# Optimization experiments

Hardware: AMD Instinct MI355X
Metric: run time of the kernel (lower is better)

Reference implementation:

```python
import jax, jax.numpy as jnp
import numpy as np

IN_C, OUT_C = 32, 64
KSIZE = (3, 3, 3)


def setup_inputs() -> dict:
    key = jax.random.key(0)
    k1, k2 = jax.random.split(key)
    x = jax.random.normal(k1, (2, IN_C, 64, 64, 64), dtype=jnp.float32)
    # One learnable scalar per (out_channel, in_channel, kz, ky, kx) basis function.
    W = jax.random.normal(k2, (OUT_C, IN_C) + KSIZE, dtype=jnp.float32) * 0.05
    return {"x": x, "W": W}


def reference(x, W):
    # Original: for each (oc, ic, kz, ky, kx), out[:, oc] += basis(x[:, ic, shifted_slices])
    # With scalar-weight bases this is exactly a VALID (unpadded) 3D convolution:
    # out[b, o, d, h, w] = sum_{i, kz, ky, kx} W[o, i, kz, ky, kx] * x[b, i, d+kz, h+ky, w+kx]
    return jax.lax.conv_general_dilated(
        x, W,
        window_strides=(1, 1, 1),
        padding="VALID",
        dimension_numbers=("NCDHW", "OIDHW", "NCDHW"),
    )
```

## Files before the change

kernel.cpp:

```cpp
#include <hip/hip_runtime.h>
#include <hip/hip_bf16.h>

#define DIN 64
#define DOUT 62
#define ICH 32
#define OCH 64

typedef __bf16 bf16x8 __attribute__((ext_vector_type(8)));
typedef float f32x4 __attribute__((ext_vector_type(4)));
typedef float f32x8 __attribute__((ext_vector_type(8)));
typedef float f32x16 __attribute__((ext_vector_type(16)));

#define AS1U(p) ((const __attribute__((address_space(1))) unsigned int*)(p))
#define AS3U(p) ((__attribute__((address_space(3))) unsigned int*)(p))

__global__ void prep_w(const float* __restrict__ W, unsigned short* __restrict__ Wre3) {
    int idx = blockIdx.x * 256 + threadIdx.x;
    if (idx >= 27 * OCH * ICH) return;
    int j    = idx & 7;
    int lane = (idx >> 3) & 63;
    int kh   = (idx >> 9) & 1;
    int mt   = (idx >> 10) & 1;
    int tap  = idx >> 11;
    int oc   = mt * 32 + (lane & 31);
    int ic   = kh * 16 + (lane >> 5) * 8 + j;
    float v  = W[((size_t)oc * ICH + ic) * 27 + tap];
    Wre3[idx] = __builtin_bit_cast(unsigned short, (__bf16)v);
}

__global__ void prep_x(const float* __restrict__ x, unsigned short* __restrict__ xp) {
    int idx = blockIdx.x * 256 + threadIdx.x;
    int w = idx & 63;
    int s = (idx >> 6) & 3;
    int y = (idx >> 8) & 63;
    int z = (idx >> 14) & 63;
    int b = idx >> 20;
    const float* xb = x + ((size_t)(b * ICH + s * 8)) * 262144 + (size_t)z * 4096 + y * 64 + w;
    bf16x8 pk;
#pragma unroll
    for (int j = 0; j < 8; ++j)
        pk[j] = (__bf16)xb[(size_t)j * 262144];
    ((int4*)xp)[idx] = __builtin_bit_cast(int4, pk);
}

__global__ __launch_bounds__(512, 4) void conv3d_mfma_pk(
    const unsigned short* __restrict__ Wre3,
    const unsigned short* __restrict__ xp,
    float* __restrict__ out)
{
    __shared__ char xs[2][40960];

    const int tid  = threadIdx.x;
    const int lane = tid & 63;
    const int wave = tid >> 6;

    const int orig = blockIdx.x;
    const int lid  = (orig & 7) * 124 + (orig >> 3);
    const int ht = lid & 7;
    const int rr = lid >> 3;
    const int d  = rr % DOUT;
    const int b  = rr / DOUT;
    const int h0 = ht * 8;

    const int l31 = lane & 31;
    const int lhi = lane >> 5;
    const int row = wave;

    auto stage_chunk = [&](char* buf, int z, int i) {
        int c  = wave * 5 + i;
        int yl = c >> 2;
        int sl = c & 3;
        int srow = h0 + yl; if (srow > 63) srow = 63;
        const unsigned short* src =
            xp + ((((size_t)(b * DIN + z) * DIN + srow) * 4 + sl) * 64) * 8 + lane * 8;
        __builtin_amdgcn_global_load_lds(AS1U(src), AS3U(buf + c * 1024), 16, 0, 0);
    };
    auto loadA = [&](int tap, int4* af) {
        const int4* wp = (const int4*)Wre3 + (size_t)tap * 256 + lane;
#pragma unroll
        for (int q = 0; q < 4; ++q)
            af[q] = wp[q * 64];
    };
    auto readB = [&](const char* buf, int ky, int kx, int4* dst) {
#pragma unroll
        for (int kh = 0; kh < 2; ++kh) {
            const int g = kh * 2 + lhi;
#pragma unroll
            for (int nt = 0; nt < 2; ++nt) {
                int wb = nt * 32 + l31 + kx;
                if (wb > 63) wb = 63;
                dst[kh * 2 + nt] = *(const int4*)(buf + (((row + ky) * 4 + g) * 64 + wb) * 16);
            }
        }
    };

#pragma unroll
    for (int i = 0; i < 5; ++i) stage_chunk(xs[0], d, i);
    int4 af[2][4];
    loadA(0, af[0]);

    f32x16 acc[2][2];
#pragma unroll
    for (int mt = 0; mt < 2; ++mt)
#pragma unroll
        for (int nt = 0; nt < 2; ++nt)
#pragma unroll
            for (int r = 0; r < 16; ++r) acc[mt][nt][r] = 0.f;

    __syncthreads();

#pragma unroll
    for (int kz = 0; kz < 3; ++kz) {
        char* cur = xs[kz & 1];
        char* nxt = xs[(kz + 1) & 1];

#pragma unroll
        for (int t = 0; t < 9; ++t) {
            const int T = kz * 9 + t;
            int4 bfr[4];
            readB(cur, t / 3, t % 3, bfr);
            if (T < 26) loadA(T + 1, af[(T + 1) & 1]);
            if (kz < 2 && t < 5) stage_chunk(nxt, d + kz + 1, t);

            __builtin_amdgcn_s_setprio(1);
#pragma unroll
            for (int kh = 0; kh < 2; ++kh)
#pragma unroll
                for (int mt = 0; mt < 2; ++mt)
#pragma unroll
                    for (int nt = 0; nt < 2; ++nt)
                        acc[mt][nt] = __builtin_amdgcn_mfma_f32_32x32x16_bf16(
                            __builtin_bit_cast(bf16x8, af[T & 1][mt * 2 + kh]),
                            __builtin_bit_cast(bf16x8, bfr[kh * 2 + nt]),
                            acc[mt][nt], 0, 0, 0);
            __builtin_amdgcn_s_setprio(0);
        }
        if (kz < 2) __syncthreads();
    }

    const int h = h0 + row;
    if (h < DOUT) {
#pragma unroll
        for (int mt = 0; mt < 2; ++mt) {
#pragma unroll
            for (int r = 0; r < 16; ++r) {
                int oc = mt * 32 + (r & 3) + 8 * (r >> 2) + 4 * lhi;
                size_t ob = ((((size_t)b * OCH + oc) * DOUT + d) * DOUT + h) * DOUT;
#pragma unroll
                for (int nt = 0; nt < 2; ++nt) {
                    int ww = nt * 32 + l31;
                    if (ww < DOUT) out[ob + ww] = acc[mt][nt][r];
                }
            }
        }
    }
}

__global__ __launch_bounds__(256, 3) void conv3d_mfma_fb(
    const float* __restrict__ x, const float* __restrict__ W,
    float* __restrict__ out)
{
    __shared__ char xs[2][6 * 66 * 64];

    const int tid  = threadIdx.x;
    const int lane = tid & 63;
    const int wave = tid >> 6;

    const int orig = blockIdx.x;
    const int lid  = (orig & 7) * 248 + (orig >> 3);
    const int ht = lid & 15;
    const int rr = lid >> 4;
    const int d  = rr % DOUT;
    const int b  = rr / DOUT;
    const int h0 = ht * 4;

    const int wlo = lane & 15;
    const int whi = lane >> 4;
    const int row = wave;

    const int icg  = wave;
    const int w    = lane;
    const int slot = icg ^ ((w >> 1) & 3);

    auto issueRow = [&](int z, int y) -> f32x8 {
        int gy = h0 + y; if (gy > 63) gy = 63;
        const float* xp2 = x + (((size_t)(b * ICH + icg * 8) * DIN + z) * DIN + gy) * DIN + w;
        f32x8 s;
#pragma unroll
        for (int j = 0; j < 8; ++j) s[j] = xp2[(size_t)j * DIN * DIN * DIN];
        return s;
    };
    auto writeRow = [&](char* buf, int y, f32x8 s) {
        bf16x8 pk;
#pragma unroll
        for (int j = 0; j < 8; ++j) pk[j] = (__bf16)s[j];
        *(int4*)(buf + ((y * 66 + w) * 64 + slot * 16)) = __builtin_bit_cast(int4, pk);
    };
    auto loadA = [&](int tap, int4* af) {
#pragma unroll
        for (int mt = 0; mt < 4; ++mt) {
            const float* wp = W + ((size_t)(mt * 16 + wlo) * ICH + whi * 8) * 27 + tap;
            bf16x8 t;
#pragma unroll
            for (int j = 0; j < 8; ++j) t[j] = (__bf16)wp[j * 27];
            af[mt] = __builtin_bit_cast(int4, t);
        }
    };
    auto readB = [&](const char* buf, int ky, int kx, int4* dst) {
#pragma unroll
        for (int nt = 0; nt < 4; ++nt) {
            int wb = nt * 16 + wlo + kx;
            int sl = whi ^ ((wb >> 1) & 3);
            dst[nt] = *(const int4*)(buf + (((row + ky) * 66 + wb) * 64 + sl * 16));
        }
    };

    if (tid < 96) {
        int bu = tid / 48, q2 = tid % 48;
        int y = q2 >> 3, q = q2 & 7;
        int w2 = 64 + (q >> 2), sl = q & 3;
        *(int4*)(xs[bu] + ((y * 66 + w2) * 64 + sl * 16)) = int4{0, 0, 0, 0};
    }
    {
        f32x8 s0 = issueRow(d, 0), s1 = issueRow(d, 1), s2 = issueRow(d, 2);
        writeRow(xs[0], 0, s0); s0 = issueRow(d, 3);
        writeRow(xs[0], 1, s1); s1 = issueRow(d, 4);
        writeRow(xs[0], 2, s2); s2 = issueRow(d, 5);
        writeRow(xs[0], 3, s0); writeRow(xs[0], 4, s1); writeRow(xs[0], 5, s2);
    }
    int4 af[2][4];
    loadA(0, af[0]);
    __syncthreads();

    f32x4 acc[4][4];
#pragma unroll
    for (int mt = 0; mt < 4; ++mt)
#pragma unroll
        for (int nt = 0; nt < 4; ++nt)
            acc[mt][nt] = f32x4{0.f, 0.f, 0.f, 0.f};

    int4 bfr[2][4];

#pragma unroll
    for (int kz = 0; kz < 3; ++kz) {
        char* cur = xs[kz & 1];
        char* nxt = xs[(kz + 1) & 1];
        f32x8 s0, s1, s2;
        readB(cur, 0, 0, bfr[0]);
#pragma unroll
        for (int t = 0; t < 9; ++t) {
            const int T = kz * 9 + t;
            if (T < 26) loadA(T + 1, af[(T + 1) & 1]);
            if (t < 8)  readB(cur, (t + 1) / 3, (t + 1) % 3, bfr[(t + 1) & 1]);
            if (kz < 2) {
                if (t == 3) writeRow(nxt, 0, s0);
                if (t == 4) writeRow(nxt, 1, s1);
                if (t == 5) writeRow(nxt, 2, s2);
                if (t == 6) writeRow(nxt, 3, s0);
                if (t == 7) writeRow(nxt, 4, s1);
                if (t == 8) writeRow(nxt, 5, s2);
                if (t == 0) s0 = issueRow(d + kz + 1, 0);
                if (t == 1) s1 = issueRow(d + kz + 1, 1);
                if (t == 2) s2 = issueRow(d + kz + 1, 2);
                if (t == 3) s0 = issueRow(d + kz + 1, 3);
                if (t == 4) s1 = issueRow(d + kz + 1, 4);
                if (t == 5) s2 = issueRow(d + kz + 1, 5);
            }
#pragma unroll
            for (int mt = 0; mt < 4; ++mt)
#pragma unroll
                for (int nt = 0; nt < 4; ++nt)
                    acc[mt][nt] = __builtin_amdgcn_mfma_f32_16x16x32_bf16(
                        __builtin_bit_cast(bf16x8, af[T & 1][mt]),
                        __builtin_bit_cast(bf16x8, bfr[t & 1][nt]),
                        acc[mt][nt], 0, 0, 0);
        }
        if (kz < 2) __syncthreads();
    }

    const int h = h0 + row;
    if (h < DOUT) {
#pragma unroll
        for (int mt = 0; mt < 4; ++mt) {
#pragma unroll
            for (int r = 0; r < 4; ++r) {
                int oc = mt * 16 + whi * 4 + r;
                size_t ob = ((((size_t)b * OCH + oc) * DOUT + d) * DOUT + h) * DOUT;
#pragma unroll
                for (int nt = 0; nt < 4; ++nt) {
                    int ww = nt * 16 + wlo;
                    if (ww < DOUT) out[ob + ww] = acc[mt][nt][r];
                }
            }
        }
    }
}

extern "C" void kernel_launch(void* const* d_in, const int* in_sizes, int n_in,
                              void* d_out, int out_size, void* d_ws, size_t ws_size,
                              hipStream_t stream) {
    const float* x = (const float*)d_in[0];
    const float* W = (const float*)d_in[1];
    float* out = (float*)d_out;

    const size_t wre_elems = (size_t)27 * OCH * ICH;
    const size_t xp_elems  = (size_t)2 * DIN * DIN * DIN * ICH;
    const size_t need = (wre_elems + xp_elems) * 2 + 256;

    if (ws_size >= need) {
        unsigned short* Wre3 = (unsigned short*)d_ws;
        unsigned short* xp   = Wre3 + wre_elems;
        prep_w<<<216, 256, 0, stream>>>(W, Wre3);
        prep_x<<<8192, 256, 0, stream>>>(x, xp);
        conv3d_mfma_pk<<<dim3(2 * DOUT * 8), 512, 0, stream>>>(Wre3, xp, out);
    } else {
        conv3d_mfma_fb<<<dim3(2 * DOUT * 16), 256, 0, stream>>>(x, W, out);
    }
}
```

Before: 90.26 us.

## Halve per-block tile to 4 rows, split width across waves, double-buffer B reads

Each block now covers 4 output rows instead of 8, with the 8 waves split into 4 rows by 2 width halves. That halves the per-wave accumulators and B registers, cuts LDS per block from 80KB to 48KB, and doubles the grid, with launch bounds raised to allow more resident blocks per CU. It also prefetches the next tap's B fragments into a double buffer so LDS reads overlap the MFMAs. The cost is more halo rows staged per output row (6 rows per 4 outputs instead of 10 per 8) and each weight fragment is reused across only one width tile per wave.

```diff
diff --git a/kernel.cpp b/kernel.cpp
--- a/kernel.cpp
+++ b/kernel.cpp
@@ -43,31 +43,32 @@
     ((int4*)xp)[idx] = __builtin_bit_cast(int4, pk);
 }
 
-__global__ __launch_bounds__(512, 4) void conv3d_mfma_pk(
+__global__ __launch_bounds__(512, 6) void conv3d_mfma_pk(
     const unsigned short* __restrict__ Wre3,
     const unsigned short* __restrict__ xp,
     float* __restrict__ out)
 {
-    __shared__ char xs[2][40960];
+    __shared__ char xs[2][24576];
 
     const int tid  = threadIdx.x;
     const int lane = tid & 63;
     const int wave = tid >> 6;
+    const int row  = wave & 3;
+    const int whalf= wave >> 2;
 
     const int orig = blockIdx.x;
-    const int lid  = (orig & 7) * 124 + (orig >> 3);
-    const int ht = lid & 7;
-    const int rr = lid >> 3;
+    const int lid  = (orig & 7) * 248 + (orig >> 3);
+    const int ht = lid & 15;
+    const int rr = lid >> 4;
     const int d  = rr % DOUT;
     const int b  = rr / DOUT;
-    const int h0 = ht * 8;
+    const int h0 = ht * 4;
 
     const int l31 = lane & 31;
     const int lhi = lane >> 5;
-    const int row = wave;
 
     auto stage_chunk = [&](char* buf, int z, int i) {
-        int c  = wave * 5 + i;
+        int c  = wave * 3 + i;
         int yl = c >> 2;
         int sl = c & 3;
         int srow = h0 + yl; if (srow > 63) srow = 63;
@@ -82,75 +83,66 @@
             af[q] = wp[q * 64];
     };
     auto readB = [&](const char* buf, int ky, int kx, int4* dst) {
+        int wb = whalf * 32 + l31 + kx;
+        if (wb > 63) wb = 63;
 #pragma unroll
         for (int kh = 0; kh < 2; ++kh) {
             const int g = kh * 2 + lhi;
-#pragma unroll
-            for (int nt = 0; nt < 2; ++nt) {
-                int wb = nt * 32 + l31 + kx;
-                if (wb > 63) wb = 63;
-                dst[kh * 2 + nt] = *(const int4*)(buf + (((row + ky) * 4 + g) * 64 + wb) * 16);
-            }
-        }
-    };
-
-#pragma unroll
-    for (int i = 0; i < 5; ++i) stage_chunk(xs[0], d, i);
+            dst[kh] = *(const int4*)(buf + (((row + ky) * 4 + g) * 64 + wb) * 16);
+        }
+    };
+
+#pragma unroll
+    for (int i = 0; i < 3; ++i) stage_chunk(xs[0], d, i);
     int4 af[2][4];
     loadA(0, af[0]);
 
-    f32x16 acc[2][2];
+    f32x16 acc[2];
 #pragma unroll
     for (int mt = 0; mt < 2; ++mt)
 #pragma unroll
-        for (int nt = 0; nt < 2; ++nt)
-#pragma unroll
-            for (int r = 0; r < 16; ++r) acc[mt][nt][r] = 0.f;
+        for (int r = 0; r < 16; ++r) acc[mt][r] = 0.f;
 
     __syncthreads();
+
+    int4 bfr[2][2];
 
 #pragma unroll
     for (int kz = 0; kz < 3; ++kz) {
         char* cur = xs[kz & 1];
         char* nxt = xs[(kz + 1) & 1];
+        readB(cur, 0, 0, bfr[0]);
 
 #pragma unroll
         for (int t = 0; t < 9; ++t) {
             const int T = kz * 9 + t;
-            int4 bfr[4];
-            readB(cur, t / 3, t % 3, bfr);
             if (T < 26) loadA(T + 1, af[(T + 1) & 1]);
-            if (kz < 2 && t < 5) stage_chunk(nxt, d + kz + 1, t);
+            if (t < 8)  readB(cur, (t + 1) / 3, (t + 1) % 3, bfr[(t + 1) & 1]);
+            if (kz < 2 && t < 3) stage_chunk(nxt, d + kz + 1, t);
 
             __builtin_amdgcn_s_setprio(1);
 #pragma unroll
             for (int kh = 0; kh < 2; ++kh)
 #pragma unroll
                 for (int mt = 0; mt < 2; ++mt)
-#pragma unroll
-                    for (int nt = 0; nt < 2; ++nt)
-                        acc[mt][nt] = __builtin_amdgcn_mfma_f32_32x32x16_bf16(
-                            __builtin_bit_cast(bf16x8, af[T & 1][mt * 2 + kh]),
-                            __builtin_bit_cast(bf16x8, bfr[kh * 2 + nt]),
-                            acc[mt][nt], 0, 0, 0);
+                    acc[mt] = __builtin_amdgcn_mfma_f32_32x32x16_bf16(
+                        __builtin_bit_cast(bf16x8, af[T & 1][mt * 2 + kh]),
+                        __builtin_bit_cast(bf16x8, bfr[t & 1][kh]),
+                        acc[mt], 0, 0, 0);
             __builtin_amdgcn_s_setprio(0);
         }
         if (kz < 2) __syncthreads();
     }
 
     const int h = h0 + row;
-    if (h < DOUT) {
+    const int ww = whalf * 32 + l31;
+    if (h < DOUT && ww < DOUT) {
 #pragma unroll
         for (int mt = 0; mt < 2; ++mt) {
 #pragma unroll
             for (int r = 0; r < 16; ++r) {
                 int oc = mt * 32 + (r & 3) + 8 * (r >> 2) + 4 * lhi;
-                size_t ob = ((((size_t)b * OCH + oc) * DOUT + d) * DOUT + h) * DOUT;
-#pragma unroll
-                for (int nt = 0; nt < 2; ++nt) {
-                    int ww = nt * 32 + l31;
-                    if (ww < DOUT) out[ob + ww] = acc[mt][nt][r];
-                }
+                out[((((size_t)b * OCH + oc) * DOUT + d) * DOUT + h) * DOUT + ww] = acc[mt][r];
             }
         }
     }
@@ -312,7 +304,7 @@
         unsigned short* xp   = Wre3 + wre_elems;
         prep_w<<<216, 256, 0, stream>>>(W, Wre3);
         prep_x<<<8192, 256, 0, stream>>>(x, xp);
-        conv3d_mfma_pk<<<dim3(2 * DOUT * 8), 512, 0, stream>>>(Wre3, xp, out);
+        conv3d_mfma_pk<<<dim3(2 * DOUT * 16), 512, 0, stream>>>(Wre3, xp, out);
     } else {
         conv3d_mfma_fb<<<dim3(2 * DOUT * 16), 256, 0, stream>>>(x, W, out);
     }
```

Result: slower. 300.0 us (+232.4%).

## Drop LDS staging; read conv input directly from global with register prefetch

Applied to the files above, without the earlier changes.

Removes the double-buffered LDS staging of input rows via global_load_lds and the block barriers. Each wave now loads its B fragments directly from the packed bf16 input in global memory, prefetching two taps ahead in a 3-deep register ring. Blocks shrink to 256 threads covering 4 output rows, with twice as many blocks. This is meant to eliminate barrier stalls and LDS traffic, at the cost of redundant global and L2 reads across overlapping rows and taps, and higher register pressure.

```diff
diff --git a/kernel.cpp b/kernel.cpp
--- a/kernel.cpp
+++ b/kernel.cpp
@@ -10,9 +10,6 @@
 typedef float f32x4 __attribute__((ext_vector_type(4)));
 typedef float f32x8 __attribute__((ext_vector_type(8)));
 typedef float f32x16 __attribute__((ext_vector_type(16)));
-
-#define AS1U(p) ((const __attribute__((address_space(1))) unsigned int*)(p))
-#define AS3U(p) ((__attribute__((address_space(3))) unsigned int*)(p))
 
 __global__ void prep_w(const float* __restrict__ W, unsigned short* __restrict__ Wre3) {
     int idx = blockIdx.x * 256 + threadIdx.x;
@@ -43,61 +40,51 @@
     ((int4*)xp)[idx] = __builtin_bit_cast(int4, pk);
 }
 
-__global__ __launch_bounds__(512, 4) void conv3d_mfma_pk(
+__global__ __launch_bounds__(256, 3) void conv3d_mfma_pk(
     const unsigned short* __restrict__ Wre3,
     const unsigned short* __restrict__ xp,
     float* __restrict__ out)
 {
-    __shared__ char xs[2][40960];
-
     const int tid  = threadIdx.x;
     const int lane = tid & 63;
     const int wave = tid >> 6;
 
     const int orig = blockIdx.x;
-    const int lid  = (orig & 7) * 124 + (orig >> 3);
-    const int ht = lid & 7;
-    const int rr = lid >> 3;
+    const int lid  = (orig & 7) * 248 + (orig >> 3);
+    const int ht = lid & 15;
+    const int rr = lid >> 4;
     const int d  = rr % DOUT;
     const int b  = rr / DOUT;
-    const int h0 = ht * 8;
+    const int h0 = ht * 4;
 
     const int l31 = lane & 31;
     const int lhi = lane >> 5;
     const int row = wave;
 
-    auto stage_chunk = [&](char* buf, int z, int i) {
-        int c  = wave * 5 + i;
-        int yl = c >> 2;
-        int sl = c & 3;
-        int srow = h0 + yl; if (srow > 63) srow = 63;
-        const unsigned short* src =
-            xp + ((((size_t)(b * DIN + z) * DIN + srow) * 4 + sl) * 64) * 8 + lane * 8;
-        __builtin_amdgcn_global_load_lds(AS1U(src), AS3U(buf + c * 1024), 16, 0, 0);
-    };
     auto loadA = [&](int tap, int4* af) {
         const int4* wp = (const int4*)Wre3 + (size_t)tap * 256 + lane;
 #pragma unroll
         for (int q = 0; q < 4; ++q)
             af[q] = wp[q * 64];
     };
-    auto readB = [&](const char* buf, int ky, int kx, int4* dst) {
+    auto readB = [&](int z, int ky, int kx, int4* dst) {
+        int y = h0 + row + ky; if (y > 63) y = 63;
+        const int4* base = (const int4*)xp + ((((size_t)b * DIN + z) * DIN + y) * 4) * 64;
+        int w0 = l31 + kx;
+        int w1 = 32 + l31 + kx; if (w1 > 63) w1 = 63;
 #pragma unroll
         for (int kh = 0; kh < 2; ++kh) {
             const int g = kh * 2 + lhi;
-#pragma unroll
-            for (int nt = 0; nt < 2; ++nt) {
-                int wb = nt * 32 + l31 + kx;
-                if (wb > 63) wb = 63;
-                dst[kh * 2 + nt] = *(const int4*)(buf + (((row + ky) * 4 + g) * 64 + wb) * 16);
-            }
-        }
-    };
-
-#pragma unroll
-    for (int i = 0; i < 5; ++i) stage_chunk(xs[0], d, i);
+            dst[kh * 2 + 0] = base[g * 64 + w0];
+            dst[kh * 2 + 1] = base[g * 64 + w1];
+        }
+    };
+
     int4 af[2][4];
+    int4 bfr[3][4];
     loadA(0, af[0]);
+    readB(d, 0, 0, bfr[0]);
+    readB(d, 0, 1, bfr[1]);
 
     f32x16 acc[2][2];
 #pragma unroll
@@ -107,35 +94,26 @@
 #pragma unroll
             for (int r = 0; r < 16; ++r) acc[mt][nt][r] = 0.f;
 
-    __syncthreads();
-
-#pragma unroll
-    for (int kz = 0; kz < 3; ++kz) {
-        char* cur = xs[kz & 1];
-        char* nxt = xs[(kz + 1) & 1];
-
-#pragma unroll
-        for (int t = 0; t < 9; ++t) {
-            const int T = kz * 9 + t;
-            int4 bfr[4];
-            readB(cur, t / 3, t % 3, bfr);
-            if (T < 26) loadA(T + 1, af[(T + 1) & 1]);
-            if (kz < 2 && t < 5) stage_chunk(nxt, d + kz + 1, t);
-
-            __builtin_amdgcn_s_setprio(1);
-#pragma unroll
-            for (int kh = 0; kh < 2; ++kh)
-#pragma unroll
-                for (int mt = 0; mt < 2; ++mt)
-#pragma unroll
-                    for (int nt = 0; nt < 2; ++nt)
-                        acc[mt][nt] = __builtin_amdgcn_mfma_f32_32x32x16_bf16(
-                            __builtin_bit_cast(bf16x8, af[T & 1][mt * 2 + kh]),
-                            __builtin_bit_cast(bf16x8, bfr[kh * 2 + nt]),
-                            acc[mt][nt], 0, 0, 0);
-            __builtin_amdgcn_s_setprio(0);
-        }
-        if (kz < 2) __syncthreads();
+#pragma unroll
+    for (int T = 0; T < 27; ++T) {
+        if (T < 26) loadA(T + 1, af[(T + 1) & 1]);
+        if (T < 25) {
+            const int Tn = T + 2;
+            readB(d + Tn / 9, (Tn % 9) / 3, Tn % 3, bfr[Tn % 3]);
+        }
+
+        __builtin_amdgcn_s_setprio(1);
+#pragma unroll
+        for (int kh = 0; kh < 2; ++kh)
+#pragma unroll
+            for (int mt = 0; mt < 2; ++mt)
+#pragma unroll
+                for (int nt = 0; nt < 2; ++nt)
+                    acc[mt][nt] = __builtin_amdgcn_mfma_f32_32x32x16_bf16(
+                        __builtin_bit_cast(bf16x8, af[T & 1][mt * 2 + kh]),
+                        __builtin_bit_cast(bf16x8, bfr[T % 3][kh * 2 + nt]),
+                        acc[mt][nt], 0, 0, 0);
+        __builtin_amdgcn_s_setprio(0);
     }
 
     const int h = h0 + row;
@@ -312,7 +290,7 @@
         unsigned short* xp   = Wre3 + wre_elems;
         prep_w<<<216, 256, 0, stream>>>(W, Wre3);
         prep_x<<<8192, 256, 0, stream>>>(x, xp);
-        conv3d_mfma_pk<<<dim3(2 * DOUT * 8), 512, 0, stream>>>(Wre3, xp, out);
+        conv3d_mfma_pk<<<dim3(2 * DOUT * 16), 256, 0, stream>>>(Wre3, xp, out);
     } else {
         conv3d_mfma_fb<<<dim3(2 * DOUT * 16), 256, 0, stream>>>(x, W, out);
     }
```

After: 139.4 us. 54.4% more time.

## Compute two output rows per wave to reuse weight fragments across rows

Applied to the files above, without the earlier changes.

Halves the block to 4 waves, and each wave now computes two adjacent output rows. Each weight A-fragment load therefore feeds twice as many MFMAs, which halves global weight-load traffic per output. Each wave stages 10 input chunks instead of 5, and the s_setprio hints are removed. The cost is double the accumulator registers (64 f32x16 values' worth), which lowers occupancy to the declared 2 blocks of 256 per CU, and fewer waves are available to hide latency.

```diff
diff --git a/kernel.cpp b/kernel.cpp
--- a/kernel.cpp
+++ b/kernel.cpp
@@ -43,7 +43,7 @@
     ((int4*)xp)[idx] = __builtin_bit_cast(int4, pk);
 }
 
-__global__ __launch_bounds__(512, 4) void conv3d_mfma_pk(
+__global__ __launch_bounds__(256, 2) void conv3d_mfma_pk(
     const unsigned short* __restrict__ Wre3,
     const unsigned short* __restrict__ xp,
     float* __restrict__ out)
@@ -64,10 +64,10 @@
 
     const int l31 = lane & 31;
     const int lhi = lane >> 5;
-    const int row = wave;
+    const int row0 = wave * 2;
 
     auto stage_chunk = [&](char* buf, int z, int i) {
-        int c  = wave * 5 + i;
+        int c  = wave * 10 + i;
         int yl = c >> 2;
         int sl = c & 3;
         int srow = h0 + yl; if (srow > 63) srow = 63;
@@ -81,7 +81,7 @@
         for (int q = 0; q < 4; ++q)
             af[q] = wp[q * 64];
     };
-    auto readB = [&](const char* buf, int ky, int kx, int4* dst) {
+    auto readB = [&](const char* buf, int yloc, int kx, int4* dst) {
 #pragma unroll
         for (int kh = 0; kh < 2; ++kh) {
             const int g = kh * 2 + lhi;
@@ -89,25 +89,29 @@
             for (int nt = 0; nt < 2; ++nt) {
                 int wb = nt * 32 + l31 + kx;
                 if (wb > 63) wb = 63;
-                dst[kh * 2 + nt] = *(const int4*)(buf + (((row + ky) * 4 + g) * 64 + wb) * 16);
-            }
-        }
-    };
-
-#pragma unroll
-    for (int i = 0; i < 5; ++i) stage_chunk(xs[0], d, i);
+                dst[kh * 2 + nt] = *(const int4*)(buf + ((yloc * 4 + g) * 64 + wb) * 16);
+            }
+        }
+    };
+
+#pragma unroll
+    for (int i = 0; i < 10; ++i) stage_chunk(xs[0], d, i);
     int4 af[2][4];
     loadA(0, af[0]);
 
-    f32x16 acc[2][2];
-#pragma unroll
-    for (int mt = 0; mt < 2; ++mt)
-#pragma unroll
-        for (int nt = 0; nt < 2; ++nt)
-#pragma unroll
-            for (int r = 0; r < 16; ++r) acc[mt][nt][r] = 0.f;
+    f32x16 acc[2][2][2];
+#pragma unroll
+    for (int r2 = 0; r2 < 2; ++r2)
+#pragma unroll
+        for (int mt = 0; mt < 2; ++mt)
+#pragma unroll
+            for (int nt = 0; nt < 2; ++nt)
+#pragma unroll
+                for (int r = 0; r < 16; ++r) acc[r2][mt][nt][r] = 0.f;
 
     __syncthreads();
+
+    int4 bfr0[4], bfr1[4];
 
 #pragma unroll
     for (int kz = 0; kz < 3; ++kz) {
@@ -116,40 +120,56 @@
 
 #pragma unroll
         for (int t = 0; t < 9; ++t) {
-            const int T = kz * 9 + t;
-            int4 bfr[4];
-            readB(cur, t / 3, t % 3, bfr);
+            const int T  = kz * 9 + t;
+            const int ky = t / 3, kx = t % 3;
+
+            readB(cur, row0 + ky, kx, bfr0);
             if (T < 26) loadA(T + 1, af[(T + 1) & 1]);
-            if (kz < 2 && t < 5) stage_chunk(nxt, d + kz + 1, t);
-
-            __builtin_amdgcn_s_setprio(1);
+            if (kz < 2) {
+                if (t == 0) { stage_chunk(nxt, d + kz + 1, 0); stage_chunk(nxt, d + kz + 1, 1); }
+                else        { stage_chunk(nxt, d + kz + 1, t + 1); }
+            }
+            readB(cur, row0 + 1 + ky, kx, bfr1);
+
 #pragma unroll
             for (int kh = 0; kh < 2; ++kh)
 #pragma unroll
                 for (int mt = 0; mt < 2; ++mt)
 #pragma unroll
                     for (int nt = 0; nt < 2; ++nt)
-                        acc[mt][nt] = __builtin_amdgcn_mfma_f32_32x32x16_bf16(
+                        acc[0][mt][nt] = __builtin_amdgcn_mfma_f32_32x32x16_bf16(
                             __builtin_bit_cast(bf16x8, af[T & 1][mt * 2 + kh]),
-                            __builtin_bit_cast(bf16x8, bfr[kh * 2 + nt]),
-                            acc[mt][nt], 0, 0, 0);
-            __builtin_amdgcn_s_setprio(0);
+                            __builtin_bit_cast(bf16x8, bfr0[kh * 2 + nt]),
+                            acc[0][mt][nt], 0, 0, 0);
+#pragma unroll
+            for (int kh = 0; kh < 2; ++kh)
+#pragma unroll
+                for (int mt = 0; mt < 2; ++mt)
+#pragma unroll
+                    for (int nt = 0; nt < 2; ++nt)
+                        acc[1][mt][nt] = __builtin_amdgcn_mfma_f32_32x32x16_bf16(
+                            __builtin_bit_cast(bf16x8, af[T & 1][mt * 2 + kh]),
+                            __builtin_bit_cast(bf16x8, bfr1[kh * 2 + nt]),
+                            acc[1][mt][nt], 0, 0, 0);
         }
         if (kz < 2) __syncthreads();
     }
 
-    const int h = h0 + row;
-    if (h < DOUT) {
-#pragma unroll
-        for (int mt = 0; mt < 2; ++mt) {
-#pragma unroll
-            for (int r = 0; r < 16; ++r) {
-                int oc = mt * 32 + (r & 3) + 8 * (r >> 2) + 4 * lhi;
-                size_t ob = ((((size_t)b * OCH + oc) * DOUT + d) * DOUT + h) * DOUT;
-#pragma unroll
-                for (int nt = 0; nt < 2; ++nt) {
-                    int ww = nt * 32 + l31;
-                    if (ww < DOUT) out[ob + ww] = acc[mt][nt][r];
+#pragma unroll
+    for (int r2 = 0; r2 < 2; ++r2) {
+        const int h = h0 + row0 + r2;
+        if (h < DOUT) {
+#pragma unroll
+            for (int mt = 0; mt < 2; ++mt) {
+#pragma unroll
+                for (int r = 0; r < 16; ++r) {
+                    int oc = mt * 32 + (r & 3) + 8 * (r >> 2) + 4 * lhi;
+                    size_t ob = ((((size_t)b * OCH + oc) * DOUT + d) * DOUT + h) * DOUT;
+#pragma unroll
+                    for (int nt = 0; nt < 2; ++nt) {
+                        int ww = nt * 32 + l31;
+                        if (ww < DOUT) out[ob + ww] = acc[r2][mt][nt][r];
+                    }
                 }
             }
         }
@@ -312,7 +332,7 @@
         unsigned short* xp   = Wre3 + wre_elems;
         prep_w<<<216, 256, 0, stream>>>(W, Wre3);
         prep_x<<<8192, 256, 0, stream>>>(x, xp);
-        conv3d_mfma_pk<<<dim3(2 * DOUT * 8), 512, 0, stream>>>(Wre3, xp, out);
+        conv3d_mfma_pk<<<dim3(2 * DOUT * 8), 256, 0, stream>>>(Wre3, xp, out);
     } else {
         conv3d_mfma_fb<<<dim3(2 * DOUT * 16), 256, 0, stream>>>(x, W, out);
     }
```

Result: faster. 87.17 us (-3.4%).
